# Kernel optimization log

Measured on AMD Instinct MI355X. Metric: run time of the kernel, lower is better.

The kernel has to match this reference:

```python
import jax, jax.numpy as jnp
import numpy as np
import math

D_MODEL = 1024
NUM_HEADS = 16
D_K = D_MODEL // NUM_HEADS
B, S = 2, 2048


def _linear_weight(key, out_f, in_f):
    return jax.random.normal(key, (out_f, in_f), jnp.float32) * math.sqrt(2.0 / in_f)


def setup_inputs() -> dict:
    key = jax.random.key(0)
    ks = jax.random.split(key, 5)
    x = jax.random.normal(ks[0], (B, S, D_MODEL), jnp.float32)
    return {
        "x": x,
        "Wq": _linear_weight(ks[1], D_MODEL, D_MODEL),
        "bq": jnp.zeros((D_MODEL,), jnp.float32),
        "Wk": _linear_weight(ks[2], D_MODEL, D_MODEL),
        "bk": jnp.zeros((D_MODEL,), jnp.float32),
        "Wv": _linear_weight(ks[3], D_MODEL, D_MODEL),
        "bv": jnp.zeros((D_MODEL,), jnp.float32),
        "Wo": _linear_weight(ks[4], D_MODEL, D_MODEL),
        "bo": jnp.zeros((D_MODEL,), jnp.float32),
    }


def reference(x, Wq, bq, Wk, bk, Wv, bv, Wo, bo):
    b, s, _ = x.shape
    # Projections: x @ W.T + b (CustomLinear stores weight as (out, in))
    q = jnp.einsum("bsd,ed->bse", x, Wq) + bq
    k = jnp.einsum("bsd,ed->bse", x, Wk) + bk
    v = jnp.einsum("bsd,ed->bse", x, Wv) + bv
    # (b, h, s, d_k)
    q = q.reshape(b, s, NUM_HEADS, D_K).transpose(0, 2, 1, 3)
    k = k.reshape(b, s, NUM_HEADS, D_K).transpose(0, 2, 1, 3)
    v = v.reshape(b, s, NUM_HEADS, D_K).transpose(0, 2, 1, 3)
    # Scaled dot-product attention with fully materialized scores (faithful)
    scores = jnp.einsum("bhqd,bhkd->bhqk", q, k) / math.sqrt(D_K)
    attn = jax.nn.softmax(scores, axis=-1)
    out = jnp.einsum("bhqk,bhkd->bhqd", attn, v)
    out = out.transpose(0, 2, 1, 3).reshape(b, s, D_MODEL)
    return jnp.einsum("bsd,ed->bse", out, Wo) + bo
```

## Files before the change

### kernel.cpp

```cpp
#include <hip/hip_runtime.h>
#include <hip/hip_bf16.h>

using bf16 = __hip_bfloat16;
typedef __attribute__((ext_vector_type(8))) short short8;
typedef __attribute__((ext_vector_type(4))) short s4v;
typedef __attribute__((ext_vector_type(4))) float float4v;
typedef __attribute__((ext_vector_type(4))) float f32x4;

#define MFMA16(a, b, c) __builtin_amdgcn_mfma_f32_16x16x32_bf16((a), (b), (c), 0, 0, 0)

#define GLD_LDS16(g, l)                                            \
    __builtin_amdgcn_global_load_lds(                              \
        (const __attribute__((address_space(1))) void*)(g),        \
        (__attribute__((address_space(3))) void*)(l), 16, 0, 0)

constexpr int Bc = 2;
constexpr int Sc = 2048;
constexpr int Hc = 16;
constexpr int DKc = 64;
constexpr int Dc = 1024;
constexpr size_t MEG = 1024 * 1024;

union BFU { bf16 h; short s; };

__device__ inline short bfbits(float f) {
    BFU u; u.h = __float2bfloat16(f); return u.s;
}

__device__ inline short8 load_cvt8(const float* __restrict__ p) {
    f32x4 a = *(const f32x4*)p;
    f32x4 b = *(const f32x4*)(p + 4);
    short8 r;
    r[0] = bfbits(a[0]); r[1] = bfbits(a[1]); r[2] = bfbits(a[2]); r[3] = bfbits(a[3]);
    r[4] = bfbits(b[0]); r[5] = bfbits(b[1]); r[6] = bfbits(b[2]); r[7] = bfbits(b[3]);
    return r;
}

__global__ __launch_bounds__(256) void cvt_kernel(
    const float* __restrict__ x, const float* __restrict__ Wq,
    const float* __restrict__ Wk, const float* __restrict__ Wv,
    const float* __restrict__ Wo, bf16* __restrict__ dst)
{
    const size_t i = ((size_t)blockIdx.x * 256 + threadIdx.x) * 8;
    const float* s;
    if      (i < 4 * MEG) s = x  + i;
    else if (i < 5 * MEG) s = Wq + (i - 4 * MEG);
    else if (i < 6 * MEG) s = Wk + (i - 5 * MEG);
    else if (i < 7 * MEG) s = Wv + (i - 6 * MEG);
    else                  s = Wo + (i - 7 * MEG);
    *(short8*)(dst + i) = load_cvt8(s);
}

__global__ __launch_bounds__(256) void qkv_gemm_kernel(
    const bf16* __restrict__ x,
    const bf16* __restrict__ Wq, const float* __restrict__ bq,
    const bf16* __restrict__ Wk, const float* __restrict__ bk,
    const bf16* __restrict__ Wv, const float* __restrict__ bv,
    bf16* __restrict__ q_ws, bf16* __restrict__ k_ws, bf16* __restrict__ v_ws)
{
    constexpr int BM = 128, BN = 128, BK = 32;
    __shared__ __align__(16) bf16 sA[BM * BK];
    __shared__ __align__(16) bf16 sB[BN * BK];

    const int bx = blockIdx.x;
    const int sel = bx >> 3;
    const int n0 = (bx & 7) * BN;
    const int m0 = blockIdx.y * BM;

    const bf16* __restrict__ Wsel = (sel == 0) ? Wq : ((sel == 1) ? Wk : Wv);
    const float* __restrict__ bsel = (sel == 0) ? bq : ((sel == 1) ? bk : bv);

    const int t = threadIdx.x;
    const int lane = t & 63;
    const int wave = t >> 6;
    const int ln = lane & 15;
    const int qd = lane >> 4;
    const int wm = (wave >> 1) * 64;
    const int wn = (wave & 1) * 64;

    const int gr = lane >> 2;
    const int gc = (lane & 3) * 8;

    float4v acc[4][4];
#pragma unroll
    for (int i = 0; i < 4; i++)
#pragma unroll
        for (int j = 0; j < 4; j++) acc[i][j] = (float4v)0.0f;

    for (int kk = 0; kk < Dc; kk += BK) {
        __syncthreads();
#pragma unroll
        for (int cc = 0; cc < 2; cc++) {
            const int c = wave * 2 + cc;
            GLD_LDS16(x    + (size_t)(m0 + c * 16 + gr) * Dc + kk + gc, &sA[c * 512]);
            GLD_LDS16(Wsel + (size_t)(n0 + c * 16 + gr) * Dc + kk + gc, &sB[c * 512]);
        }
        __syncthreads();

        short8 af[4], wf[4];
#pragma unroll
        for (int i = 0; i < 4; i++)
            af[i] = *(const short8*)&sA[(wm + i * 16 + ln) * BK + qd * 8];
#pragma unroll
        for (int j = 0; j < 4; j++)
            wf[j] = *(const short8*)&sB[(wn + j * 16 + ln) * BK + qd * 8];
#pragma unroll
        for (int i = 0; i < 4; i++)
#pragma unroll
            for (int j = 0; j < 4; j++)
                acc[i][j] = MFMA16(af[i], wf[j], acc[i][j]);
    }

    constexpr float QSCALE = 0.125f * 1.44269504088896f;

#pragma unroll
    for (int j = 0; j < 4; j++) {
        const int n = n0 + wn + j * 16 + ln;
        const float bias = bsel[n];
        const int h_ = n >> 6, d_ = n & 63;
#pragma unroll
        for (int i = 0; i < 4; i++) {
            const int mbase = m0 + wm + i * 16 + qd * 4;
            if (sel == 2) {
                const int b_ = mbase >> 11, s_ = mbase & 2047;
                s4v pk;
#pragma unroll
                for (int r = 0; r < 4; r++)
                    pk[r] = bfbits(acc[i][j][r] + bias);
                *(s4v*)&v_ws[(((size_t)(b_ * Hc + h_)) * DKc + d_) * Sc + s_] = pk;
            } else {
#pragma unroll
                for (int r = 0; r < 4; r++) {
                    const int m = mbase + r;
                    const int b_ = m >> 11, s_ = m & 2047;
                    float v = acc[i][j][r] + bias;
                    if (sel == 0) v *= QSCALE;
                    const bf16 o = __float2bfloat16(v);
                    if (sel == 0)
                        q_ws[(((size_t)(b_ * Hc + h_)) * Sc + s_) * DKc + d_] = o;
                    else
                        k_ws[(((size_t)(b_ * Hc + h_)) * Sc + s_) * DKc + d_] = o;
                }
            }
        }
    }
}

__global__ __launch_bounds__(512) void attn_kernel(
    const bf16* __restrict__ q_ws, const bf16* __restrict__ k_ws,
    const bf16* __restrict__ v_ws, bf16* __restrict__ ao_ws)
{
    constexpr int LQP = 76;
    __shared__ __align__(16) bf16 sQ[128 * 64];
    __shared__ __align__(16) bf16 sK[2][64 * 64];
    __shared__ __align__(16) bf16 sV[2][64 * 64];
    __shared__ __align__(16) short sP[8][16 * LQP];

    const int bh = blockIdx.x;
    const int qt = blockIdx.y;
    const int t = threadIdx.x;
    const int lane = t & 63;
    const int wave = t >> 6;
    const int ln = lane & 15;
    const int qd = lane >> 4;
    short* const sPw = sP[wave];

    const bf16* __restrict__ Qbase = q_ws + (size_t)bh * Sc * DKc + qt * 128 * DKc;
    const bf16* __restrict__ Kbase = k_ws + (size_t)bh * Sc * DKc;
    const bf16* __restrict__ Vbase = v_ws + (size_t)bh * DKc * Sc;

    const int rloc = lane >> 3;
    const int blk = lane & 7;

    {
#pragma unroll
        for (int cc = 0; cc < 2; cc++) {
            const int c = wave * 2 + cc;
            const int row = c * 8 + rloc;
            const int gb = blk ^ (row & 7);
            GLD_LDS16(Qbase + (size_t)row * DKc + gb * 8, &sQ[c * 512]);
        }
    }
    {
        const int row = wave * 8 + rloc;
        const int gb = blk ^ (row & 7);
        GLD_LDS16(Kbase + (size_t)row * DKc + gb * 8, &sK[0][wave * 512]);
        GLD_LDS16(Vbase + (size_t)row * Sc + gb * 8, &sV[0][wave * 512]);
    }

    short8 ones8;
    {
        const short ob = (ln == 0) ? (short)0x3F80 : (short)0;
#pragma unroll
        for (int i = 0; i < 8; i++) ones8[i] = ob;
    }

    float4v oacc[5];
#pragma unroll
    for (int j = 0; j < 5; j++) oacc[j] = (float4v)0.0f;

    for (int kt = 0; kt < Sc / 64; kt++) {
        const int cur = kt & 1;
        __syncthreads();
        if (kt + 1 < Sc / 64) {
            const int nxt = (kt + 1) & 1;
            const int row = wave * 8 + rloc;
            const int gb = blk ^ (row & 7);
            GLD_LDS16(Kbase + (size_t)((kt + 1) * 64 + row) * DKc + gb * 8,
                      &sK[nxt][wave * 512]);
            GLD_LDS16(Vbase + (size_t)row * Sc + (kt + 1) * 64 + gb * 8,
                      &sV[nxt][wave * 512]);
        }

        float4v sacc[4];
#pragma unroll
        for (int j = 0; j < 4; j++) sacc[j] = (float4v)0.0f;
#pragma unroll
        for (int ks = 0; ks < 2; ks++) {
            const int qrow = wave * 16 + ln;
            const short8 bq = *(const short8*)
                &sQ[qrow * 64 + (((ks * 4 + qd) ^ (qrow & 7)) << 3)];
#pragma unroll
            for (int j = 0; j < 4; j++) {
                const int row = j * 16 + ln;
                const short8 ak = *(const short8*)
                    &sK[cur][row * 64 + (((ks * 4 + qd) ^ (row & 7)) << 3)];
                sacc[j] = MFMA16(ak, bq, sacc[j]);
            }
        }

#pragma unroll
        for (int j = 0; j < 4; j++) {
            s4v pk;
#pragma unroll
            for (int r = 0; r < 4; r++)
                pk[r] = bfbits(exp2f(sacc[j][r]));
            *(s4v*)&sPw[ln * LQP + j * 16 + qd * 4] = pk;
        }

#pragma unroll
        for (int ks = 0; ks < 2; ks++) {
            const s4v p0 = *(const s4v*)&sPw[ln * LQP + ks * 32 + qd * 8];
            const s4v p1 = *(const s4v*)&sPw[ln * LQP + ks * 32 + qd * 8 + 4];
            short8 ap;
            ap[0] = p0[0]; ap[1] = p0[1]; ap[2] = p0[2]; ap[3] = p0[3];
            ap[4] = p1[0]; ap[5] = p1[1]; ap[6] = p1[2]; ap[7] = p1[3];
#pragma unroll
            for (int j = 0; j < 4; j++) {
                const int row = j * 16 + ln;
                const short8 bv_ = *(const short8*)
                    &sV[cur][row * 64 + (((ks * 4 + qd) ^ (row & 7)) << 3)];
                oacc[j] = MFMA16(ap, bv_, oacc[j]);
            }
            oacc[4] = MFMA16(ap, ones8, oacc[4]);
        }
    }

    const int b_ = bh >> 4, h_ = bh & 15;
#pragma unroll
    for (int r = 0; r < 4; r++) {
        const float l = __shfl(oacc[4][r], lane & 48, 64);
        const float inv = 1.0f / l;
        const int s_ = qt * 128 + wave * 16 + qd * 4 + r;
#pragma unroll
        for (int j = 0; j < 4; j++) {
            const int d_ = j * 16 + ln;
            ao_ws[(((size_t)(b_ * Sc + s_)) * Hc + h_) * DKc + d_] =
                __float2bfloat16(oacc[j][r] * inv);
        }
    }
}

__global__ __launch_bounds__(256) void out_gemm_kernel(
    const bf16* __restrict__ A, const bf16* __restrict__ Wo,
    const float* __restrict__ bo, float* __restrict__ out)
{
    constexpr int BM = 128, BN = 128, BK = 32;
    __shared__ __align__(16) bf16 sA[BM * BK];
    __shared__ __align__(16) bf16 sB[BN * BK];

    const int n0 = blockIdx.x * BN;
    const int m0 = blockIdx.y * BM;

    const int t = threadIdx.x;
    const int lane = t & 63;
    const int wave = t >> 6;
    const int ln = lane & 15;
    const int qd = lane >> 4;
    const int wm = (wave >> 1) * 64;
    const int wn = (wave & 1) * 64;

    const int gr = lane >> 2;
    const int gc = (lane & 3) * 8;

    float4v acc[4][4];
#pragma unroll
    for (int i = 0; i < 4; i++)
#pragma unroll
        for (int j = 0; j < 4; j++) acc[i][j] = (float4v)0.0f;

    for (int kk = 0; kk < Dc; kk += BK) {
        __syncthreads();
#pragma unroll
        for (int cc = 0; cc < 2; cc++) {
            const int c = wave * 2 + cc;
            GLD_LDS16(A  + (size_t)(m0 + c * 16 + gr) * Dc + kk + gc, &sA[c * 512]);
            GLD_LDS16(Wo + (size_t)(n0 + c * 16 + gr) * Dc + kk + gc, &sB[c * 512]);
        }
        __syncthreads();

        short8 af[4], wf[4];
#pragma unroll
        for (int i = 0; i < 4; i++)
            af[i] = *(const short8*)&sA[(wm + i * 16 + ln) * BK + qd * 8];
#pragma unroll
        for (int j = 0; j < 4; j++)
            wf[j] = *(const short8*)&sB[(wn + j * 16 + ln) * BK + qd * 8];
#pragma unroll
        for (int i = 0; i < 4; i++)
#pragma unroll
            for (int j = 0; j < 4; j++)
                acc[i][j] = MFMA16(af[i], wf[j], acc[i][j]);
    }

#pragma unroll
    for (int j = 0; j < 4; j++) {
        const int n = n0 + wn + j * 16 + ln;
        const float bias = bo[n];
#pragma unroll
        for (int i = 0; i < 4; i++) {
            const int mbase = m0 + wm + i * 16 + qd * 4;
#pragma unroll
            for (int r = 0; r < 4; r++) {
                const int m = mbase + r;
                out[(size_t)m * Dc + n] = acc[i][j][r] + bias;
            }
        }
    }
}

extern "C" void kernel_launch(void* const* d_in, const int* in_sizes, int n_in,
                              void* d_out, int out_size, void* d_ws, size_t ws_size,
                              hipStream_t stream)
{
    const float* x  = (const float*)d_in[0];
    const float* Wq = (const float*)d_in[1];
    const float* bq = (const float*)d_in[2];
    const float* Wk = (const float*)d_in[3];
    const float* bk = (const float*)d_in[4];
    const float* Wv = (const float*)d_in[5];
    const float* bv = (const float*)d_in[6];
    const float* Wo = (const float*)d_in[7];
    const float* bo = (const float*)d_in[8];
    float* out = (float*)d_out;

    bf16* base  = (bf16*)d_ws;
    bf16* q_ws  = base;
    bf16* k_ws  = base + 4 * MEG;
    bf16* v_ws  = base + 8 * MEG;
    bf16* ao_ws = base + 12 * MEG;
    bf16* xb    = base + 16 * MEG;
    bf16* wqb   = base + 20 * MEG;
    bf16* wkb   = base + 21 * MEG;
    bf16* wvb   = base + 22 * MEG;
    bf16* wob   = base + 23 * MEG;

    cvt_kernel<<<dim3(4096), 256, 0, stream>>>(x, Wq, Wk, Wv, Wo, xb);
    qkv_gemm_kernel<<<dim3(24, 32), 256, 0, stream>>>(
        xb, wqb, bq, wkb, bk, wvb, bv, q_ws, k_ws, v_ws);
    attn_kernel<<<dim3(32, 16), 512, 0, stream>>>(q_ws, k_ws, v_ws, ao_ws);
    out_gemm_kernel<<<dim3(8, 32), 256, 0, stream>>>(ao_ws, wob, bo, out);
}
```

Before: 201.2 us.

## Process 32 query rows per wave with Q in registers, 4 waves per block

The attention kernel now uses 4 waves of 256 threads instead of 8, and each wave handles 32 query rows (two 16-row tiles) instead of 16. Each K and V fragment read from LDS is reused for two MFMAs, which halves LDS read traffic per unit of compute. Q fragments are loaded straight from global memory into registers instead of being staged in shared memory. In exchange, register use rises and there are fewer waves per block to hide latency, since each wave must also issue twice the K/V prefetch loads.

```diff
diff --git a/kernel.cpp b/kernel.cpp
--- a/kernel.cpp
+++ b/kernel.cpp
@@ -146,15 +146,14 @@
     }
 }
 
-__global__ __launch_bounds__(512) void attn_kernel(
+__global__ __launch_bounds__(256) void attn_kernel(
     const bf16* __restrict__ q_ws, const bf16* __restrict__ k_ws,
     const bf16* __restrict__ v_ws, bf16* __restrict__ ao_ws)
 {
     constexpr int LQP = 76;
-    __shared__ __align__(16) bf16 sQ[128 * 64];
     __shared__ __align__(16) bf16 sK[2][64 * 64];
     __shared__ __align__(16) bf16 sV[2][64 * 64];
-    __shared__ __align__(16) short sP[8][16 * LQP];
+    __shared__ __align__(16) short sP[4][32 * LQP];
 
     const int bh = blockIdx.x;
     const int qt = blockIdx.y;
@@ -172,20 +171,23 @@
     const int rloc = lane >> 3;
     const int blk = lane & 7;
 
+    short8 qf[2][2];
+#pragma unroll
+    for (int nt = 0; nt < 2; nt++)
+#pragma unroll
+        for (int ks = 0; ks < 2; ks++)
+            qf[nt][ks] = *(const short8*)
+                (Qbase + (size_t)(wave * 32 + nt * 16 + ln) * DKc + ks * 32 + qd * 8);
+
     {
 #pragma unroll
         for (int cc = 0; cc < 2; cc++) {
             const int c = wave * 2 + cc;
             const int row = c * 8 + rloc;
             const int gb = blk ^ (row & 7);
-            GLD_LDS16(Qbase + (size_t)row * DKc + gb * 8, &sQ[c * 512]);
-        }
-    }
-    {
-        const int row = wave * 8 + rloc;
-        const int gb = blk ^ (row & 7);
-        GLD_LDS16(Kbase + (size_t)row * DKc + gb * 8, &sK[0][wave * 512]);
-        GLD_LDS16(Vbase + (size_t)row * Sc + gb * 8, &sV[0][wave * 512]);
+            GLD_LDS16(Kbase + (size_t)row * DKc + gb * 8, &sK[0][c * 512]);
+            GLD_LDS16(Vbase + (size_t)row * Sc + gb * 8, &sV[0][c * 512]);
+        }
     }
 
     short8 ones8;
@@ -195,80 +197,102 @@
         for (int i = 0; i < 8; i++) ones8[i] = ob;
     }
 
-    float4v oacc[5];
-#pragma unroll
-    for (int j = 0; j < 5; j++) oacc[j] = (float4v)0.0f;
+    float4v oacc[2][4];
+    float4v den[2];
+#pragma unroll
+    for (int mt = 0; mt < 2; mt++) {
+        den[mt] = (float4v)0.0f;
+#pragma unroll
+        for (int j = 0; j < 4; j++) oacc[mt][j] = (float4v)0.0f;
+    }
 
     for (int kt = 0; kt < Sc / 64; kt++) {
         const int cur = kt & 1;
         __syncthreads();
         if (kt + 1 < Sc / 64) {
             const int nxt = (kt + 1) & 1;
-            const int row = wave * 8 + rloc;
-            const int gb = blk ^ (row & 7);
-            GLD_LDS16(Kbase + (size_t)((kt + 1) * 64 + row) * DKc + gb * 8,
-                      &sK[nxt][wave * 512]);
-            GLD_LDS16(Vbase + (size_t)row * Sc + (kt + 1) * 64 + gb * 8,
-                      &sV[nxt][wave * 512]);
-        }
-
-        float4v sacc[4];
-#pragma unroll
-        for (int j = 0; j < 4; j++) sacc[j] = (float4v)0.0f;
+#pragma unroll
+            for (int cc = 0; cc < 2; cc++) {
+                const int c = wave * 2 + cc;
+                const int row = c * 8 + rloc;
+                const int gb = blk ^ (row & 7);
+                GLD_LDS16(Kbase + (size_t)((kt + 1) * 64 + row) * DKc + gb * 8,
+                          &sK[nxt][c * 512]);
+                GLD_LDS16(Vbase + (size_t)row * Sc + (kt + 1) * 64 + gb * 8,
+                          &sV[nxt][c * 512]);
+            }
+        }
+
+        float4v sacc[2][4];
+#pragma unroll
+        for (int nt = 0; nt < 2; nt++)
+#pragma unroll
+            for (int m = 0; m < 4; m++) sacc[nt][m] = (float4v)0.0f;
 #pragma unroll
         for (int ks = 0; ks < 2; ks++) {
-            const int qrow = wave * 16 + ln;
-            const short8 bq = *(const short8*)
-                &sQ[qrow * 64 + (((ks * 4 + qd) ^ (qrow & 7)) << 3)];
-#pragma unroll
-            for (int j = 0; j < 4; j++) {
-                const int row = j * 16 + ln;
+#pragma unroll
+            for (int m = 0; m < 4; m++) {
+                const int row = m * 16 + ln;
                 const short8 ak = *(const short8*)
                     &sK[cur][row * 64 + (((ks * 4 + qd) ^ (row & 7)) << 3)];
-                sacc[j] = MFMA16(ak, bq, sacc[j]);
-            }
-        }
-
-#pragma unroll
-        for (int j = 0; j < 4; j++) {
-            s4v pk;
-#pragma unroll
-            for (int r = 0; r < 4; r++)
-                pk[r] = bfbits(exp2f(sacc[j][r]));
-            *(s4v*)&sPw[ln * LQP + j * 16 + qd * 4] = pk;
-        }
+                sacc[0][m] = MFMA16(ak, qf[0][ks], sacc[0][m]);
+                sacc[1][m] = MFMA16(ak, qf[1][ks], sacc[1][m]);
+            }
+        }
+
+#pragma unroll
+        for (int nt = 0; nt < 2; nt++)
+#pragma unroll
+            for (int m = 0; m < 4; m++) {
+                s4v pk;
+#pragma unroll
+                for (int r = 0; r < 4; r++)
+                    pk[r] = bfbits(exp2f(sacc[nt][m][r]));
+                *(s4v*)&sPw[(nt * 16 + ln) * LQP + m * 16 + qd * 4] = pk;
+            }
 
 #pragma unroll
         for (int ks = 0; ks < 2; ks++) {
-            const s4v p0 = *(const s4v*)&sPw[ln * LQP + ks * 32 + qd * 8];
-            const s4v p1 = *(const s4v*)&sPw[ln * LQP + ks * 32 + qd * 8 + 4];
-            short8 ap;
-            ap[0] = p0[0]; ap[1] = p0[1]; ap[2] = p0[2]; ap[3] = p0[3];
-            ap[4] = p1[0]; ap[5] = p1[1]; ap[6] = p1[2]; ap[7] = p1[3];
+            short8 ap[2];
+#pragma unroll
+            for (int mt = 0; mt < 2; mt++) {
+                const s4v p0 = *(const s4v*)
+                    &sPw[(mt * 16 + ln) * LQP + ks * 32 + qd * 8];
+                const s4v p1 = *(const s4v*)
+                    &sPw[(mt * 16 + ln) * LQP + ks * 32 + qd * 8 + 4];
+                ap[mt][0] = p0[0]; ap[mt][1] = p0[1];
+                ap[mt][2] = p0[2]; ap[mt][3] = p0[3];
+                ap[mt][4] = p1[0]; ap[mt][5] = p1[1];
+                ap[mt][6] = p1[2]; ap[mt][7] = p1[3];
+            }
 #pragma unroll
             for (int j = 0; j < 4; j++) {
                 const int row = j * 16 + ln;
                 const short8 bv_ = *(const short8*)
                     &sV[cur][row * 64 + (((ks * 4 + qd) ^ (row & 7)) << 3)];
-                oacc[j] = MFMA16(ap, bv_, oacc[j]);
-            }
-            oacc[4] = MFMA16(ap, ones8, oacc[4]);
+                oacc[0][j] = MFMA16(ap[0], bv_, oacc[0][j]);
+                oacc[1][j] = MFMA16(ap[1], bv_, oacc[1][j]);
+            }
+            den[0] = MFMA16(ap[0], ones8, den[0]);
+            den[1] = MFMA16(ap[1], ones8, den[1]);
         }
     }
 
     const int b_ = bh >> 4, h_ = bh & 15;
 #pragma unroll
-    for (int r = 0; r < 4; r++) {
-        const float l = __shfl(oacc[4][r], lane & 48, 64);
-        const float inv = 1.0f / l;
-        const int s_ = qt * 128 + wave * 16 + qd * 4 + r;
-#pragma unroll
-        for (int j = 0; j < 4; j++) {
-            const int d_ = j * 16 + ln;
-            ao_ws[(((size_t)(b_ * Sc + s_)) * Hc + h_) * DKc + d_] =
-                __float2bfloat16(oacc[j][r] * inv);
-        }
-    }
+    for (int mt = 0; mt < 2; mt++)
+#pragma unroll
+        for (int r = 0; r < 4; r++) {
+            const float l = __shfl(den[mt][r], lane & 48, 64);
+            const float inv = 1.0f / l;
+            const int s_ = qt * 128 + wave * 32 + mt * 16 + qd * 4 + r;
+#pragma unroll
+            for (int j = 0; j < 4; j++) {
+                const int d_ = j * 16 + ln;
+                ao_ws[(((size_t)(b_ * Sc + s_)) * Hc + h_) * DKc + d_] =
+                    __float2bfloat16(oacc[mt][j][r] * inv);
+            }
+        }
 }
 
 __global__ __launch_bounds__(256) void out_gemm_kernel(
@@ -368,6 +392,6 @@
     cvt_kernel<<<dim3(4096), 256, 0, stream>>>(x, Wq, Wk, Wv, Wo, xb);
     qkv_gemm_kernel<<<dim3(24, 32), 256, 0, stream>>>(
         xb, wqb, bq, wkb, bk, wvb, bv, q_ws, k_ws, v_ws);
-    attn_kernel<<<dim3(32, 16), 512, 0, stream>>>(q_ws, k_ws, v_ws, ao_ws);
+    attn_kernel<<<dim3(32, 16), 256, 0, stream>>>(q_ws, k_ws, v_ws, ao_ws);
     out_gemm_kernel<<<dim3(8, 32), 256, 0, stream>>>(ao_ws, wob, bo, out);
 }
```

Result: slower. 208.4 us (+3.6%).
